# Kernel optimization log

Hardware: AMD Instinct MI355X
Metric: run time of the kernel (lower is better)

Reference implementation:

```python
import jax, jax.numpy as jnp
import numpy as np
from jax import lax

EPS = 1e-8  # numerical safety in squash sqrt (torch repo uses plain sqrt)

def squash(s, axis=-1):
    sq = jnp.sum(s * s, axis=axis, keepdims=True)
    return (sq / (1.0 + sq)) * s / jnp.sqrt(sq + EPS)

def conv2d(x, w, b, stride):
    y = lax.conv_general_dilated(x, w, (stride, stride), 'VALID',
                                 dimension_numbers=('NCHW', 'OIHW', 'NCHW'))
    return y + b[None, :, None, None]

def setup_inputs() -> dict:
    key = jax.random.key(0)
    ks = jax.random.split(key, 12)
    B = 256
    x = jax.random.normal(ks[0], (B, 1, 28, 28), dtype=jnp.float32)
    conv_w = jax.random.normal(ks[1], (256, 1, 9, 9), dtype=jnp.float32) * 0.05
    conv_b = jnp.zeros((256,), dtype=jnp.float32)
    caps1_w = jax.random.normal(ks[2], (32, 8, 256, 9, 9), dtype=jnp.float32) * 0.01
    caps1_b = jnp.zeros((32, 8), dtype=jnp.float32)
    caps2_w = jax.random.normal(ks[3], (10, 1152, 8, 16), dtype=jnp.float32)  # torch.randn
    dec_w1 = jax.random.normal(ks[4], (160, 512), dtype=jnp.float32) * 0.05
    dec_b1 = jnp.zeros((512,), dtype=jnp.float32)
    dec_w2 = jax.random.normal(ks[5], (512, 1024), dtype=jnp.float32) * 0.04
    dec_b2 = jnp.zeros((1024,), dtype=jnp.float32)
    dec_w3 = jax.random.normal(ks[6], (1024, 784), dtype=jnp.float32) * 0.03
    dec_b3 = jnp.zeros((784,), dtype=jnp.float32)
    return {"x": x, "conv_w": conv_w, "conv_b": conv_b, "caps1_w": caps1_w,
            "caps1_b": caps1_b, "caps2_w": caps2_w, "dec_w1": dec_w1,
            "dec_b1": dec_b1, "dec_w2": dec_w2, "dec_b2": dec_b2,
            "dec_w3": dec_w3, "dec_b3": dec_b3}

def reference(x, conv_w, conv_b, caps1_w, caps1_b, caps2_w,
              dec_w1, dec_b1, dec_w2, dec_b2, dec_w3, dec_b3):
    B = x.shape[0]
    # conv + relu -> [B,256,20,20]
    h = jax.nn.relu(conv2d(x, conv_w, conv_b, 1))
    # CapsLayerOne: 32 parallel convs folded into one grouped-out conv -> [B,256,6,6]
    u = conv2d(h, caps1_w.reshape(32 * 8, 256, 9, 9), caps1_b.reshape(-1), 2)
    u = u.reshape(B, 32, 8, 6, 6)                    # [B,caps,ch,h,w]
    # replicate torch cat(dim=-1).view(B,8,-1): flatten order (h, caps, w) per channel
    u = u.transpose(0, 2, 3, 1, 4).reshape(B, 8, 1152)  # [B,8,N]
    u = squash(u.transpose(0, 2, 1))                 # [B,N,8], N=1152
    # CapsLayerTwo dynamic routing
    x_hat = jnp.einsum('bni,cnio->cbno', u, caps2_w)[:, :, :, None, :]  # [10,B,N,1,16]
    b = jnp.zeros_like(x_hat)
    v = None
    for i in range(3):
        c = jax.nn.softmax(b, axis=2)
        s = jnp.sum(x_hat * c, axis=2, keepdims=True)  # [10,B,1,1,16]
        v = squash(s)
        if i != 2:
            b = b + jnp.sum(x_hat * v, axis=-1, keepdims=True)
    v = v[:, :, 0, 0, :].transpose(1, 0, 2)            # [B,10,16]
    class_scores = jnp.sqrt(jnp.sum(v * v, axis=-1) + EPS)  # [B,10]
    class_probabilities = jax.nn.softmax(class_scores, axis=-1)
    labels = jnp.argmax(class_probabilities, axis=1)
    y = jax.nn.one_hot(labels, 10, dtype=v.dtype)
    masked = (v * y[:, :, None]).reshape(B, 160)
    d = jax.nn.relu(masked @ dec_w1 + dec_b1)
    d = jax.nn.relu(d @ dec_w2 + dec_b2)
    reconstructions = jax.nn.sigmoid(d @ dec_w3 + dec_b3)  # [B,784]
    return (class_probabilities, reconstructions)
```

## Files before the change

### kernel.cpp

```cpp
#include <hip/hip_runtime.h>
#include <cstdint>
#include <cstddef>

#define EPSF 1e-8f

typedef __attribute__((ext_vector_type(8))) short bf16x8;
typedef __attribute__((ext_vector_type(4))) float f32x4;
typedef unsigned short ushort_t;

static __device__ __forceinline__ ushort_t f2bf(float f) {
  unsigned u = __builtin_bit_cast(unsigned, f);
  unsigned r = (u + 0x7FFFu + ((u >> 16) & 1u)) >> 16;
  return (ushort_t)r;
}
static __device__ __forceinline__ float bf2f(ushort_t h) {
  return __builtin_bit_cast(float, (unsigned)h << 16);
}

__global__ __launch_bounds__(256) void conv1_kernel(
    const float* __restrict__ x, const float* __restrict__ cw,
    const float* __restrict__ cb, ushort_t* __restrict__ h2x)
{
  int oy = blockIdx.x, b = blockIdx.y, ci = threadIdx.x;
  float w[81];
#pragma unroll
  for (int i = 0; i < 81; ++i) w[i] = cw[ci * 81 + i];
  float bias = cb[ci];
  float acc[20];
#pragma unroll
  for (int ox = 0; ox < 20; ++ox) acc[ox] = bias;
  const float* xb = x + (size_t)b * 784;
  for (int ky = 0; ky < 9; ++ky) {
    const float* row = xb + (oy + ky) * 28;
    float rv[28];
#pragma unroll
    for (int c = 0; c < 28; ++c) rv[c] = row[c];
#pragma unroll
    for (int kx = 0; kx < 9; ++kx) {
      float wv = w[ky * 9 + kx];
#pragma unroll
      for (int ox = 0; ox < 20; ++ox)
        acc[ox] = fmaf(rv[ox + kx], wv, acc[ox]);
    }
  }
  int cblk = ci >> 5, jj = ci & 31;
#pragma unroll
  for (int ox = 0; ox < 20; ++ox) {
    float a = fmaxf(acc[ox], 0.f);
    ushort_t hi = f2bf(a);
    ushort_t lo = f2bf(a - bf2f(hi));
    size_t o = ((size_t)(oy * 20 + ox) * 256 + b) * 512 + cblk * 64 + jj;
    h2x[o] = hi; h2x[o + 32] = lo;
  }
}

__global__ __launch_bounds__(256) void w2k_prep_kernel(
    const float* __restrict__ c1w, ushort_t* __restrict__ w2k)
{
  int co = blockIdx.x, ci = threadIdx.x;
  const float* src = c1w + ((size_t)co * 256 + ci) * 81;
  int cblk = ci >> 5, jj = ci & 31;
  for (int tap = 0; tap < 81; ++tap) {
    float v = src[tap];
    ushort_t hi = f2bf(v);
    size_t dst = ((size_t)co * 81 + tap) * 512 + cblk * 64 + jj;
    w2k[dst] = hi;
    w2k[dst + 32] = f2bf(v - bf2f(hi));
  }
}

__global__ __launch_bounds__(256, 2) void caps1_mfma_kernel(
    const ushort_t* __restrict__ h2x, const ushort_t* __restrict__ w2k,
    float* __restrict__ partial)
{
  int bid = blockIdx.x;
  int ks = bid & 3;
  int nt = (bid >> 2) & 1;
  int kt = (bid >> 3) & 1;
  int mt = (bid >> 4) & 1;
  int pos = bid >> 5;
  int ys = pos / 6, xs = pos % 6;
  int t = threadIdx.x;
  int wid = t >> 6, lane = t & 63;
  int wr = wid >> 1, wc = wid & 1;
  int lrow = lane & 15, g = lane >> 4;

  int b0 = mt * 128, n0 = nt * 128;
  int tb    = kt ? 41 : 0;
  int ntaps = kt ? 40 : 41;
  int nht   = 2 * ntaps;

  __shared__ ushort_t lds[2][2][128 * 64];

  f32x4 acc[4][4];
#pragma unroll
  for (int i = 0; i < 4; ++i)
#pragma unroll
    for (int j = 0; j < 4; ++j) acc[i][j] = (f32x4){0.f, 0.f, 0.f, 0.f};

  int c_ = (t & 7) ^ ((t >> 3) & 7);
  size_t aRowB[4], bRow81[4];
  int ldsBase[4];
#pragma unroll
  for (int i = 0; i < 4; ++i) {
    int row = i * 32 + (t >> 3);
    aRowB[i]  = (size_t)(b0 + row) * 512 + ks * 128 + c_ * 8;
    bRow81[i] = (size_t)(n0 + row) * 81;
    ldsBase[i] = (i * 32 + wid * 8) * 64;
  }

  auto stage = [&](int j, int bufi) {
    int tap = tb + (j >> 1);
    int half = j & 1;
    int ky = tap / 9, kx = tap - ky * 9;
    int pix = (2 * ys + ky) * 20 + 2 * xs + kx;
    size_t apix = (size_t)pix * 131072 + half * 64;
    int sub = ks * 128 + half * 64 + c_ * 8;
#pragma unroll
    for (int i = 0; i < 4; ++i) {
      const ushort_t* ga = h2x + apix + aRowB[i];
      const ushort_t* gb = w2k + (bRow81[i] + tap) * 512 + sub;
      __builtin_amdgcn_global_load_lds(ga, &lds[bufi][0][ldsBase[i]], 16, 0, 0);
      __builtin_amdgcn_global_load_lds(gb, &lds[bufi][1][ldsBase[i]], 16, 0, 0);
    }
  };

  bf16x8 a_h[4], a_l[4], b_h[4], b_l[4];
  auto read_frags = [&](int bufi) {
    const ushort_t* LA = &lds[bufi][0][0];
    const ushort_t* LB = &lds[bufi][1][0];
#pragma unroll
    for (int f = 0; f < 4; ++f) {
      int ra = wr * 64 + f * 16 + lrow;
      int sa = ra * 64;
      a_h[f] = *(const bf16x8*)(LA + sa + ((g)     ^ (ra & 7)) * 8);
      a_l[f] = *(const bf16x8*)(LA + sa + ((4 + g) ^ (ra & 7)) * 8);
      int rb = wc * 64 + f * 16 + lrow;
      int sb = rb * 64;
      b_h[f] = *(const bf16x8*)(LB + sb + ((g)     ^ (rb & 7)) * 8);
      b_l[f] = *(const bf16x8*)(LB + sb + ((4 + g) ^ (rb & 7)) * 8);
    }
  };

  stage(0, 0);
  stage(1, 1);
  asm volatile("s_waitcnt vmcnt(8)" ::: "memory");
  __builtin_amdgcn_sched_barrier(0);
  __builtin_amdgcn_s_barrier();

  for (int j = 0; j < nht; ++j) {
    int cur = j & 1;
    read_frags(cur);
    asm volatile("s_waitcnt lgkmcnt(0)" ::: "memory");
    __builtin_amdgcn_sched_barrier(0);
    __builtin_amdgcn_s_barrier();

    if (j + 2 < nht) stage(j + 2, cur);
    __builtin_amdgcn_sched_barrier(0);

    __builtin_amdgcn_s_setprio(1);
#pragma unroll
    for (int mf = 0; mf < 4; ++mf)
#pragma unroll
      for (int nf = 0; nf < 4; ++nf) {
        acc[mf][nf] = __builtin_amdgcn_mfma_f32_16x16x32_bf16(a_h[mf], b_h[nf], acc[mf][nf], 0, 0, 0);
        acc[mf][nf] = __builtin_amdgcn_mfma_f32_16x16x32_bf16(a_h[mf], b_l[nf], acc[mf][nf], 0, 0, 0);
        acc[mf][nf] = __builtin_amdgcn_mfma_f32_16x16x32_bf16(a_l[mf], b_h[nf], acc[mf][nf], 0, 0, 0);
      }
    __builtin_amdgcn_s_setprio(0);
    __builtin_amdgcn_sched_barrier(0);

    if (j + 2 < nht) { asm volatile("s_waitcnt vmcnt(8)" ::: "memory"); }
    else             { asm volatile("s_waitcnt vmcnt(0)" ::: "memory"); }
    __builtin_amdgcn_sched_barrier(0);
    __builtin_amdgcn_s_barrier();
  }

  float* pp = partial + (size_t)(kt * 4 + ks) * 2359296;
#pragma unroll
  for (int mf = 0; mf < 4; ++mf) {
    int m = b0 + wr * 64 + mf * 16 + g * 4;
#pragma unroll
    for (int nf = 0; nf < 4; ++nf) {
      int n = n0 + wc * 64 + nf * 16 + lrow;
#pragma unroll
      for (int r = 0; r < 4; ++r)
        pp[((size_t)(pos * 256 + m + r)) * 256 + n] = acc[mf][nf][r];
    }
  }
}

__global__ __launch_bounds__(256) void combine_kernel(
    const float* __restrict__ partial, const float* __restrict__ c1b, float* __restrict__ u)
{
  int gidx = blockIdx.x * 256 + threadIdx.x;
  int caps = gidx & 31;
  int b = (gidx >> 5) & 255;
  int pos = gidx >> 13;
  int ys = pos / 6, xs = pos % 6;
  size_t base = ((size_t)pos * 256 + b) * 256 + caps * 8;
  f32x4 s0 = {0.f, 0.f, 0.f, 0.f}, s1 = {0.f, 0.f, 0.f, 0.f};
#pragma unroll
  for (int ksp = 0; ksp < 8; ++ksp) {
    const float* pp = partial + (size_t)ksp * 2359296 + base;
    s0 += *(const f32x4*)pp;
    s1 += *(const f32x4*)(pp + 4);
  }
  const float* bp = c1b + caps * 8;
#pragma unroll
  for (int i = 0; i < 4; ++i) { s0[i] += bp[i]; s1[i] += bp[4 + i]; }
  float sq = s0[0]*s0[0] + s0[1]*s0[1] + s0[2]*s0[2] + s0[3]*s0[3]
           + s1[0]*s1[0] + s1[1]*s1[1] + s1[2]*s1[2] + s1[3]*s1[3];
  float scale = sq / ((1.f + sq) * sqrtf(sq + EPSF));
  int nvec = ys * 192 + caps * 6 + xs;
  float* up = u + ((size_t)b * 1152 + nvec) * 8;
  f32x4 o0, o1;
#pragma unroll
  for (int i = 0; i < 4; ++i) { o0[i] = s0[i] * scale; o1[i] = s1[i] * scale; }
  *(f32x4*)up = o0;
  *(f32x4*)(up + 4) = o1;
}

__global__ __launch_bounds__(320) void xhat_kernel(
    const float* __restrict__ u, const float* __restrict__ W2, ushort_t* __restrict__ xh)
{
  int np = blockIdx.x;
  int t = threadIdx.x;
  int c  = t >> 5;
  int nh = (t >> 4) & 1;
  int o  = t & 15;
  int n = np * 2 + nh;
  __shared__ float us[2][256][8];
  for (int e = t; e < 4096; e += 320) {
    int b = e >> 4;
    int nn = (e >> 3) & 1, i = e & 7;
    us[nn][b][i] = u[((size_t)b * 1152 + np * 2 + nn) * 8 + i];
  }
  __syncthreads();
  float wcol[8];
  const float* wp = W2 + (((size_t)c * 1152 + n) * 8) * 16 + o;
#pragma unroll
  for (int i = 0; i < 8; ++i) wcol[i] = wp[i * 16];
  ushort_t* xp = xh + ((size_t)(c * 256) * 1152 + n) * 16 + o;
  for (int b = 0; b < 256; ++b) {
    float s = 0.f;
#pragma unroll
    for (int i = 0; i < 8; ++i) s = fmaf(us[nh][b][i], wcol[i], s);
    xp[(size_t)b * 18432] = f2bf(s);
  }
}

__global__ __launch_bounds__(256) void routing_kernel(
    const ushort_t* __restrict__ xhat, float* __restrict__ vout)
{
  int b = blockIdx.x, c = blockIdx.y, t = threadIdx.x;
  int wid = t >> 6, lane = t & 63;
  float xh[5][16];
  float bn[5] = {0, 0, 0, 0, 0};
  bool valid[5];
  const ushort_t* xp = xhat + ((size_t)(c * 256 + b)) * 1152 * 16;
#pragma unroll
  for (int j = 0; j < 5; ++j) {
    int n = t + 256 * j;
    valid[j] = (n < 1152);
    if (valid[j]) {
      const bf16x8* q = (const bf16x8*)(xp + (size_t)n * 16);
      bf16x8 v0 = q[0], v1 = q[1];
#pragma unroll
      for (int k = 0; k < 8; ++k) xh[j][k] = bf2f((ushort_t)v0[k]);
#pragma unroll
      for (int k = 0; k < 8; ++k) xh[j][8 + k] = bf2f((ushort_t)v1[k]);
    } else {
#pragma unroll
      for (int o = 0; o < 16; ++o) xh[j][o] = 0.f;
    }
  }
  __shared__ float redm[4], redz[4], reds[64], sv[16];
  float scale = 0.f;
  for (int it = 0; it < 3; ++it) {
    float m = -1e30f;
#pragma unroll
    for (int j = 0; j < 5; ++j) if (valid[j]) m = fmaxf(m, bn[j]);
    for (int d = 1; d < 64; d <<= 1) m = fmaxf(m, __shfl_xor(m, d));
    if (lane == 0) redm[wid] = m;
    __syncthreads();
    m = fmaxf(fmaxf(redm[0], redm[1]), fmaxf(redm[2], redm[3]));
    float e[5]; float z = 0.f;
#pragma unroll
    for (int j = 0; j < 5; ++j) { e[j] = valid[j] ? expf(bn[j] - m) : 0.f; z += e[j]; }
    for (int d = 1; d < 64; d <<= 1) z += __shfl_xor(z, d);
    if (lane == 0) redz[wid] = z;
    __syncthreads();
    z = redz[0] + redz[1] + redz[2] + redz[3];
    float ps[16];
#pragma unroll
    for (int o = 0; o < 16; ++o) ps[o] = 0.f;
#pragma unroll
    for (int j = 0; j < 5; ++j)
#pragma unroll
      for (int o = 0; o < 16; ++o) ps[o] = fmaf(e[j], xh[j][o], ps[o]);
#pragma unroll
    for (int o = 0; o < 16; ++o) {
      float vv = ps[o];
      for (int d = 1; d < 64; d <<= 1) vv += __shfl_xor(vv, d);
      if (lane == 0) reds[wid * 16 + o] = vv;
    }
    __syncthreads();
    if (t < 16) sv[t] = (reds[t] + reds[16 + t] + reds[32 + t] + reds[48 + t]) / z;
    __syncthreads();
    float vsc[16]; float sq = 0.f;
#pragma unroll
    for (int o = 0; o < 16; ++o) { vsc[o] = sv[o]; sq += sv[o] * sv[o]; }
    scale = sq / ((1.f + sq) * sqrtf(sq + EPSF));
    if (it < 2) {
#pragma unroll
      for (int j = 0; j < 5; ++j) if (valid[j]) {
        float dot = 0.f;
#pragma unroll
        for (int o = 0; o < 16; ++o) dot = fmaf(xh[j][o], vsc[o] * scale, dot);
        bn[j] += dot;
      }
    }
    __syncthreads();
  }
  if (t < 16) vout[((size_t)c * 256 + b) * 16 + t] = sv[t] * scale;
}

__global__ __launch_bounds__(256) void classify_kernel(
    const float* __restrict__ v, float* __restrict__ probs, float* __restrict__ masked)
{
  int b = blockIdx.x, t = threadIdx.x;
  __shared__ float sc[10], vv[160];
  int c = t >> 4, o = t & 15;
  float val = 0.f;
  if (t < 160) { val = v[((size_t)c * 256 + b) * 16 + o]; vv[t] = val; }
  float sq = val * val;
  sq += __shfl_xor(sq, 1); sq += __shfl_xor(sq, 2);
  sq += __shfl_xor(sq, 4); sq += __shfl_xor(sq, 8);
  if (t < 160 && o == 0) sc[c] = sqrtf(sq + EPSF);
  __syncthreads();
  float m = sc[0];
#pragma unroll
  for (int i = 1; i < 10; ++i) m = fmaxf(m, sc[i]);
  float ee[10]; float Z = 0.f;
#pragma unroll
  for (int i = 0; i < 10; ++i) { ee[i] = expf(sc[i] - m); Z += ee[i]; }
  float p[10];
#pragma unroll
  for (int i = 0; i < 10; ++i) p[i] = ee[i] / Z;
  int label = 0; float best = p[0];
#pragma unroll
  for (int i = 1; i < 10; ++i) if (p[i] > best) { best = p[i]; label = i; }
  if (t < 10) probs[(size_t)b * 10 + t] = p[t];
  if (t < 160) masked[(size_t)b * 160 + t] = (c == label) ? vv[t] : 0.f;
}

template <int ACT>
__global__ __launch_bounds__(256) void mlp_kernel(
    const float* __restrict__ A, const float* __restrict__ W,
    const float* __restrict__ bias, float* __restrict__ C, int N, int K)
{
  int j = blockIdx.x * 64 + (threadIdx.x & 63);
  int ty = threadIdx.x >> 6;
  int m0 = blockIdx.y * 16;
  __shared__ float As[16][33];
  float acc[4] = {0.f, 0.f, 0.f, 0.f};
  for (int k0 = 0; k0 < K; k0 += 32) {
    for (int e = threadIdx.x; e < 512; e += 256) {
      int r = e >> 5, kk = e & 31;
      As[r][kk] = A[(size_t)(m0 + r) * K + k0 + kk];
    }
    __syncthreads();
    if (j < N) {
      for (int kk = 0; kk < 32; ++kk) {
        float wv = W[(size_t)(k0 + kk) * N + j];
#pragma unroll
        for (int r = 0; r < 4; ++r) acc[r] = fmaf(As[ty + 4 * r][kk], wv, acc[r]);
      }
    }
    __syncthreads();
  }
  if (j < N) {
    float bv = bias[j];
#pragma unroll
    for (int r = 0; r < 4; ++r) {
      float xx = acc[r] + bv;
      if (ACT == 0) xx = fmaxf(xx, 0.f);
      else xx = 1.f / (1.f + expf(-xx));
      C[(size_t)(m0 + ty + 4 * r) * N + j] = xx;
    }
  }
}

extern "C" void kernel_launch(void* const* d_in, const int* in_sizes, int n_in,
                              void* d_out, int out_size, void* d_ws, size_t ws_size,
                              hipStream_t stream)
{
  const float* x   = (const float*)d_in[0];
  const float* cw  = (const float*)d_in[1];
  const float* cb  = (const float*)d_in[2];
  const float* c1w = (const float*)d_in[3];
  const float* c1b = (const float*)d_in[4];
  const float* c2w = (const float*)d_in[5];
  const float* w1  = (const float*)d_in[6];
  const float* b1  = (const float*)d_in[7];
  const float* w2  = (const float*)d_in[8];
  const float* b2  = (const float*)d_in[9];
  const float* w3  = (const float*)d_in[10];
  const float* b3  = (const float*)d_in[11];
  float* out = (float*)d_out;

  char* p = (char*)d_ws;
  ushort_t* xh = (ushort_t*)p;
  ushort_t* h2x = (ushort_t*)p; p += (size_t)52428800 * 2;
  ushort_t* w2k = (ushort_t*)p; p += (size_t)10616832 * 2;
  float* partial = (float*)p;   p += (size_t)8 * 2359296 * 4;
  float* u       = (float*)p;   p += (size_t)2359296 * 4;
  float* v       = (float*)p;   p += (size_t)40960 * 4;
  float* masked  = (float*)p;   p += (size_t)40960 * 4;
  float* a1      = (float*)p;   p += (size_t)131072 * 4;
  float* a2      = (float*)p;   p += (size_t)262144 * 4;

  hipLaunchKernelGGL(w2k_prep_kernel, dim3(256), dim3(256), 0, stream, c1w, w2k);
  hipLaunchKernelGGL(conv1_kernel, dim3(20, 256), dim3(256), 0, stream, x, cw, cb, h2x);
  hipLaunchKernelGGL(caps1_mfma_kernel, dim3(1152), dim3(256), 0, stream, h2x, w2k, partial);
  hipLaunchKernelGGL(combine_kernel, dim3(1152), dim3(256), 0, stream, partial, c1b, u);
  hipLaunchKernelGGL(xhat_kernel, dim3(576), dim3(320), 0, stream, u, c2w, xh);
  hipLaunchKernelGGL(routing_kernel, dim3(256, 10), dim3(256), 0, stream, xh, v);
  hipLaunchKernelGGL(classify_kernel, dim3(256), dim3(256), 0, stream, v, out, masked);
  hipLaunchKernelGGL(mlp_kernel<0>, dim3(8, 16), dim3(256), 0, stream, masked, w1, b1, a1, 512, 160);
  hipLaunchKernelGGL(mlp_kernel<0>, dim3(16, 16), dim3(256), 0, stream, a1, w2, b2, a2, 1024, 512);
  hipLaunchKernelGGL(mlp_kernel<1>, dim3(13, 16), dim3(256), 0, stream, a2, w3, b3, out + 2560, 784, 1024);
}
```

Before: 584.0 us.

## Fuse conv1 with weight prep, fold combine+squash into xhat, widen MLP grid

Measured after the change: 590.5 us. No clear change (+1.1%).

```diff
diff --git a/kernel.cpp b/kernel.cpp
--- a/kernel.cpp
+++ b/kernel.cpp
@@ -17,55 +17,55 @@
   return __builtin_bit_cast(float, (unsigned)h << 16);
 }
 
-__global__ __launch_bounds__(256) void conv1_kernel(
+__global__ __launch_bounds__(256) void conv1w2k_kernel(
     const float* __restrict__ x, const float* __restrict__ cw,
-    const float* __restrict__ cb, ushort_t* __restrict__ h2x)
-{
-  int oy = blockIdx.x, b = blockIdx.y, ci = threadIdx.x;
-  float w[81];
-#pragma unroll
-  for (int i = 0; i < 81; ++i) w[i] = cw[ci * 81 + i];
-  float bias = cb[ci];
-  float acc[20];
-#pragma unroll
-  for (int ox = 0; ox < 20; ++ox) acc[ox] = bias;
-  const float* xb = x + (size_t)b * 784;
-  for (int ky = 0; ky < 9; ++ky) {
-    const float* row = xb + (oy + ky) * 28;
-    float rv[28];
-#pragma unroll
-    for (int c = 0; c < 28; ++c) rv[c] = row[c];
-#pragma unroll
-    for (int kx = 0; kx < 9; ++kx) {
-      float wv = w[ky * 9 + kx];
-#pragma unroll
-      for (int ox = 0; ox < 20; ++ox)
-        acc[ox] = fmaf(rv[ox + kx], wv, acc[ox]);
-    }
-  }
-  int cblk = ci >> 5, jj = ci & 31;
-#pragma unroll
-  for (int ox = 0; ox < 20; ++ox) {
-    float a = fmaxf(acc[ox], 0.f);
-    ushort_t hi = f2bf(a);
-    ushort_t lo = f2bf(a - bf2f(hi));
-    size_t o = ((size_t)(oy * 20 + ox) * 256 + b) * 512 + cblk * 64 + jj;
-    h2x[o] = hi; h2x[o + 32] = lo;
-  }
-}
-
-__global__ __launch_bounds__(256) void w2k_prep_kernel(
-    const float* __restrict__ c1w, ushort_t* __restrict__ w2k)
-{
-  int co = blockIdx.x, ci = threadIdx.x;
-  const float* src = c1w + ((size_t)co * 256 + ci) * 81;
-  int cblk = ci >> 5, jj = ci & 31;
-  for (int tap = 0; tap < 81; ++tap) {
-    float v = src[tap];
-    ushort_t hi = f2bf(v);
-    size_t dst = ((size_t)co * 81 + tap) * 512 + cblk * 64 + jj;
-    w2k[dst] = hi;
-    w2k[dst + 32] = f2bf(v - bf2f(hi));
+    const float* __restrict__ cb, const float* __restrict__ c1w,
+    ushort_t* __restrict__ h2x, ushort_t* __restrict__ w2k)
+{
+  int bid = blockIdx.x, t = threadIdx.x;
+  if (bid < 5120) {
+    int oy = bid >> 8, b = bid & 255, ci = t;
+    float w[81];
+#pragma unroll
+    for (int i = 0; i < 81; ++i) w[i] = cw[ci * 81 + i];
+    float bias = cb[ci];
+    float acc[20];
+#pragma unroll
+    for (int ox = 0; ox < 20; ++ox) acc[ox] = bias;
+    const float* xb = x + (size_t)b * 784;
+    for (int ky = 0; ky < 9; ++ky) {
+      const float* row = xb + (oy + ky) * 28;
+      float rv[28];
+#pragma unroll
+      for (int c = 0; c < 28; ++c) rv[c] = row[c];
+#pragma unroll
+      for (int kx = 0; kx < 9; ++kx) {
+        float wv = w[ky * 9 + kx];
+#pragma unroll
+        for (int ox = 0; ox < 20; ++ox)
+          acc[ox] = fmaf(rv[ox + kx], wv, acc[ox]);
+      }
+    }
+    int cblk = ci >> 5, jj = ci & 31;
+#pragma unroll
+    for (int ox = 0; ox < 20; ++ox) {
+      float a = fmaxf(acc[ox], 0.f);
+      ushort_t hi = f2bf(a);
+      ushort_t lo = f2bf(a - bf2f(hi));
+      size_t o = ((size_t)(oy * 20 + ox) * 256 + b) * 512 + cblk * 64 + jj;
+      h2x[o] = hi; h2x[o + 32] = lo;
+    }
+  } else {
+    int co = bid - 5120, ci = t;
+    const float* src = c1w + ((size_t)co * 256 + ci) * 81;
+    int cblk = ci >> 5, jj = ci & 31;
+    for (int tap = 0; tap < 81; ++tap) {
+      float v = src[tap];
+      ushort_t hi = f2bf(v);
+      size_t dst = ((size_t)co * 81 + tap) * 512 + cblk * 64 + jj;
+      w2k[dst] = hi;
+      w2k[dst + 32] = f2bf(v - bf2f(hi));
+    }
   }
 }
 
@@ -190,53 +190,42 @@
   }
 }
 
-__global__ __launch_bounds__(256) void combine_kernel(
-    const float* __restrict__ partial, const float* __restrict__ c1b, float* __restrict__ u)
-{
-  int gidx = blockIdx.x * 256 + threadIdx.x;
-  int caps = gidx & 31;
-  int b = (gidx >> 5) & 255;
-  int pos = gidx >> 13;
-  int ys = pos / 6, xs = pos % 6;
-  size_t base = ((size_t)pos * 256 + b) * 256 + caps * 8;
-  f32x4 s0 = {0.f, 0.f, 0.f, 0.f}, s1 = {0.f, 0.f, 0.f, 0.f};
-#pragma unroll
-  for (int ksp = 0; ksp < 8; ++ksp) {
-    const float* pp = partial + (size_t)ksp * 2359296 + base;
-    s0 += *(const f32x4*)pp;
-    s1 += *(const f32x4*)(pp + 4);
-  }
-  const float* bp = c1b + caps * 8;
-#pragma unroll
-  for (int i = 0; i < 4; ++i) { s0[i] += bp[i]; s1[i] += bp[4 + i]; }
-  float sq = s0[0]*s0[0] + s0[1]*s0[1] + s0[2]*s0[2] + s0[3]*s0[3]
-           + s1[0]*s1[0] + s1[1]*s1[1] + s1[2]*s1[2] + s1[3]*s1[3];
-  float scale = sq / ((1.f + sq) * sqrtf(sq + EPSF));
-  int nvec = ys * 192 + caps * 6 + xs;
-  float* up = u + ((size_t)b * 1152 + nvec) * 8;
-  f32x4 o0, o1;
-#pragma unroll
-  for (int i = 0; i < 4; ++i) { o0[i] = s0[i] * scale; o1[i] = s1[i] * scale; }
-  *(f32x4*)up = o0;
-  *(f32x4*)(up + 4) = o1;
-}
-
 __global__ __launch_bounds__(320) void xhat_kernel(
-    const float* __restrict__ u, const float* __restrict__ W2, ushort_t* __restrict__ xh)
+    const float* __restrict__ partial, const float* __restrict__ c1b,
+    const float* __restrict__ W2, ushort_t* __restrict__ xh)
 {
   int np = blockIdx.x;
   int t = threadIdx.x;
-  int c  = t >> 5;
-  int nh = (t >> 4) & 1;
-  int o  = t & 15;
-  int n = np * 2 + nh;
+  int n0 = np * 2;
+  int ys = n0 / 192; int rem = n0 - ys * 192;
+  int caps = rem / 6; int xs = rem - caps * 6;
+  int pos0 = ys * 6 + xs;
   __shared__ float us[2][256][8];
   for (int e = t; e < 4096; e += 320) {
     int b = e >> 4;
     int nn = (e >> 3) & 1, i = e & 7;
-    us[nn][b][i] = u[((size_t)b * 1152 + np * 2 + nn) * 8 + i];
+    size_t base = ((size_t)((pos0 + nn) * 256 + b)) * 256 + caps * 8 + i;
+    float s = c1b[caps * 8 + i];
+#pragma unroll
+    for (int ksp = 0; ksp < 8; ++ksp) s += partial[(size_t)ksp * 2359296 + base];
+    us[nn][b][i] = s;
   }
   __syncthreads();
+  for (int pp = t; pp < 512; pp += 320) {
+    int nn = pp >> 8, b = pp & 255;
+    float* row = us[nn][b];
+    float sq = 0.f;
+#pragma unroll
+    for (int i = 0; i < 8; ++i) sq += row[i] * row[i];
+    float scale = sq / ((1.f + sq) * sqrtf(sq + EPSF));
+#pragma unroll
+    for (int i = 0; i < 8; ++i) row[i] *= scale;
+  }
+  __syncthreads();
+  int c  = t >> 5;
+  int nh = (t >> 4) & 1;
+  int o  = t & 15;
+  int n = n0 + nh;
   float wcol[8];
   const float* wp = W2 + (((size_t)c * 1152 + n) * 8) * 16 + o;
 #pragma unroll
@@ -360,11 +349,11 @@
     const float* __restrict__ A, const float* __restrict__ W,
     const float* __restrict__ bias, float* __restrict__ C, int N, int K)
 {
-  int j = blockIdx.x * 64 + (threadIdx.x & 63);
-  int ty = threadIdx.x >> 6;
+  int j = blockIdx.x * 32 + (threadIdx.x & 31);
+  int ty = threadIdx.x >> 5;
   int m0 = blockIdx.y * 16;
   __shared__ float As[16][33];
-  float acc[4] = {0.f, 0.f, 0.f, 0.f};
+  float acc[2] = {0.f, 0.f};
   for (int k0 = 0; k0 < K; k0 += 32) {
     for (int e = threadIdx.x; e < 512; e += 256) {
       int r = e >> 5, kk = e & 31;
@@ -374,8 +363,8 @@
     if (j < N) {
       for (int kk = 0; kk < 32; ++kk) {
         float wv = W[(size_t)(k0 + kk) * N + j];
-#pragma unroll
-        for (int r = 0; r < 4; ++r) acc[r] = fmaf(As[ty + 4 * r][kk], wv, acc[r]);
+        acc[0] = fmaf(As[ty][kk], wv, acc[0]);
+        acc[1] = fmaf(As[ty + 8][kk], wv, acc[1]);
       }
     }
     __syncthreads();
@@ -383,11 +372,11 @@
   if (j < N) {
     float bv = bias[j];
 #pragma unroll
-    for (int r = 0; r < 4; ++r) {
+    for (int r = 0; r < 2; ++r) {
       float xx = acc[r] + bv;
       if (ACT == 0) xx = fmaxf(xx, 0.f);
       else xx = 1.f / (1.f + expf(-xx));
-      C[(size_t)(m0 + ty + 4 * r) * N + j] = xx;
+      C[(size_t)(m0 + ty + 8 * r) * N + j] = xx;
     }
   }
 }
@@ -415,20 +404,17 @@
   ushort_t* h2x = (ushort_t*)p; p += (size_t)52428800 * 2;
   ushort_t* w2k = (ushort_t*)p; p += (size_t)10616832 * 2;
   float* partial = (float*)p;   p += (size_t)8 * 2359296 * 4;
-  float* u       = (float*)p;   p += (size_t)2359296 * 4;
   float* v       = (float*)p;   p += (size_t)40960 * 4;
   float* masked  = (float*)p;   p += (size_t)40960 * 4;
   float* a1      = (float*)p;   p += (size_t)131072 * 4;
   float* a2      = (float*)p;   p += (size_t)262144 * 4;
 
-  hipLaunchKernelGGL(w2k_prep_kernel, dim3(256), dim3(256), 0, stream, c1w, w2k);
-  hipLaunchKernelGGL(conv1_kernel, dim3(20, 256), dim3(256), 0, stream, x, cw, cb, h2x);
+  hipLaunchKernelGGL(conv1w2k_kernel, dim3(5376), dim3(256), 0, stream, x, cw, cb, c1w, h2x, w2k);
   hipLaunchKernelGGL(caps1_mfma_kernel, dim3(1152), dim3(256), 0, stream, h2x, w2k, partial);
-  hipLaunchKernelGGL(combine_kernel, dim3(1152), dim3(256), 0, stream, partial, c1b, u);
-  hipLaunchKernelGGL(xhat_kernel, dim3(576), dim3(320), 0, stream, u, c2w, xh);
+  hipLaunchKernelGGL(xhat_kernel, dim3(576), dim3(320), 0, stream, partial, c1b, c2w, xh);
   hipLaunchKernelGGL(routing_kernel, dim3(256, 10), dim3(256), 0, stream, xh, v);
   hipLaunchKernelGGL(classify_kernel, dim3(256), dim3(256), 0, stream, v, out, masked);
-  hipLaunchKernelGGL(mlp_kernel<0>, dim3(8, 16), dim3(256), 0, stream, masked, w1, b1, a1, 512, 160);
-  hipLaunchKernelGGL(mlp_kernel<0>, dim3(16, 16), dim3(256), 0, stream, a1, w2, b2, a2, 1024, 512);
-  hipLaunchKernelGGL(mlp_kernel<1>, dim3(13, 16), dim3(256), 0, stream, a2, w3, b3, out + 2560, 784, 1024);
-}
+  hipLaunchKernelGGL(mlp_kernel<0>, dim3(16, 16), dim3(256), 0, stream, masked, w1, b1, a1, 512, 160);
+  hipLaunchKernelGGL(mlp_kernel<0>, dim3(32, 16), dim3(256), 0, stream, a1, w2, b2, a2, 1024, 512);
+  hipLaunchKernelGGL(mlp_kernel<1>, dim3(25, 16), dim3(256), 0, stream, a2, w3, b3, out + 2560, 784, 1024);
+}
```
